# Kernel optimization log

Measured on AMD Instinct MI355X. Metric: run time of the kernel, lower is better.

Reference implementation:

```python
import jax, jax.numpy as jnp
import numpy as np

B, T = 32, 64
C, H, W = 1, 32, 32
A, E, D, S, HID = 2, 64, 128, 32, 128
K, STRIDE, PAD = 4, 2, 1
FEAT = 64 * 4 * 4  # conv stack output: 64 channels at 4x4


def _lin(x, w, b):
    return x @ w.T + b


def _conv(x, w, b):
    y = jax.lax.conv_general_dilated(x, w, (STRIDE, STRIDE), [(PAD, PAD)] * 2,
                                     dimension_numbers=('NCHW', 'OIHW', 'NCHW'))
    return y + b[None, :, None, None]


def _deconv(x, w, b):
    # torch ConvTranspose2d(w: (in_c,out_c,k,k), stride=2, pad=1) as dilated conv
    w_ = jnp.flip(w, (2, 3)).transpose(1, 0, 2, 3)
    p = K - 1 - PAD
    y = jax.lax.conv_general_dilated(x, w_, (1, 1), [(p, p)] * 2,
                                     lhs_dilation=(STRIDE, STRIDE),
                                     dimension_numbers=('NCHW', 'OIHW', 'NCHW'))
    return y + b[None, :, None, None]


def _mlp(x, w1, b1, w2, b2, w3, b3):
    h = jax.nn.elu(_lin(x, w1, b1))
    h = jax.nn.elu(_lin(h, w2, b2))
    out = _lin(h, w3, b3)
    return out[..., :S], jnp.clip(out[..., S:], -5.0, 2.0)


def _gru(x, h, wih, whh, bih, bhh):
    # torch nn.GRUCell semantics
    gi = x @ wih.T + bih
    gh = h @ whh.T + bhh
    ir, iz, inn = jnp.split(gi, 3, -1)
    hr, hz, hn = jnp.split(gh, 3, -1)
    r = jax.nn.sigmoid(ir + hr)
    u = jax.nn.sigmoid(iz + hz)
    n = jnp.tanh(inn + r * hn)
    return (1.0 - u) * n + u * h


def setup_inputs():
    keys = iter(jax.random.split(jax.random.key(0), 64))

    def p(shape, fan):
        return jax.random.normal(next(keys), shape, jnp.float32) / np.sqrt(fan)

    return dict(
        obs=jax.random.normal(next(keys), (B, T, C, H, W), jnp.float32),
        actions=jax.random.normal(next(keys), (B, T, A), jnp.float32),
        noise=jax.random.normal(next(keys), (T, B, S), jnp.float32),
        enc_w1=p((32, C, K, K), C * K * K), enc_b1=jnp.zeros(32),
        enc_w2=p((64, 32, K, K), 32 * K * K), enc_b2=jnp.zeros(64),
        enc_w3=p((64, 64, K, K), 64 * K * K), enc_b3=jnp.zeros(64),
        enc_pw=p((E, FEAT), FEAT), enc_pb=jnp.zeros(E),
        dec_pw=p((FEAT, D + S), D + S), dec_pb=jnp.zeros(FEAT),
        dec_w1=p((64, 64, K, K), 64 * K * K), dec_b1=jnp.zeros(64),
        dec_w2=p((64, 32, K, K), 64 * K * K), dec_b2=jnp.zeros(32),
        dec_w3=p((32, C, K, K), 32 * K * K), dec_b3=jnp.zeros(C),
        gru_wih=p((3 * D, S + A), D), gru_whh=p((3 * D, D), D),
        gru_bih=jnp.zeros(3 * D), gru_bhh=jnp.zeros(3 * D),
        pri_w1=p((HID, D + A), D + A), pri_b1=jnp.zeros(HID),
        pri_w2=p((HID, HID), HID), pri_b2=jnp.zeros(HID),
        pri_w3=p((2 * S, HID), HID), pri_b3=jnp.zeros(2 * S),
        pos_w1=p((HID, D + E), D + E), pos_b1=jnp.zeros(HID),
        pos_w2=p((HID, HID), HID), pos_b2=jnp.zeros(HID),
        pos_w3=p((2 * S, HID), HID), pos_b3=jnp.zeros(2 * S),
    )


def reference(obs, actions, noise, enc_w1, enc_b1, enc_w2, enc_b2, enc_w3, enc_b3,
              enc_pw, enc_pb, dec_pw, dec_pb, dec_w1, dec_b1, dec_w2, dec_b2,
              dec_w3, dec_b3, gru_wih, gru_whh, gru_bih, gru_bhh,
              pri_w1, pri_b1, pri_w2, pri_b2, pri_w3, pri_b3,
              pos_w1, pos_b1, pos_w2, pos_b2, pos_w3, pos_b3):
    Bq, Tq = obs.shape[:2]
    # --- CNN encoder over all frames at once ---
    x = obs.reshape(Bq * Tq, C, H, W)
    x = jax.nn.relu(_conv(x, enc_w1, enc_b1))
    x = jax.nn.relu(_conv(x, enc_w2, enc_b2))
    x = jax.nn.relu(_conv(x, enc_w3, enc_b3))
    embed = _lin(x.reshape(Bq * Tq, -1), enc_pw, enc_pb).reshape(Bq, Tq, E)

    # --- sequential RSSM core (use_posterior=True path) ---
    def step(h, inp):
        a, e_t, eps = inp
        pm, pls = _mlp(jnp.concatenate([h, e_t], -1),
                       pos_w1, pos_b1, pos_w2, pos_b2, pos_w3, pos_b3)
        z = pm + jnp.exp(pls) * eps
        prm, prls = _mlp(jnp.concatenate([h, a], -1),
                         pri_w1, pri_b1, pri_w2, pri_b2, pri_w3, pri_b3)
        h_new = _gru(jnp.concatenate([z, a], -1), h, gru_wih, gru_whh, gru_bih, gru_bhh)
        return h_new, (z, prm, prls, pm, pls, h)  # h = pre-update (used for decode)

    h0 = jnp.zeros((Bq, D), obs.dtype)
    h_final, (zs, prm, prls, pm, pls, hs) = jax.lax.scan(
        step, h0, (actions.swapaxes(0, 1), embed.swapaxes(0, 1), noise))

    # --- batched decode of all (h_t, z_t); same math as per-step decode ---
    hz = jnp.concatenate([hs, zs], -1).reshape(Tq * Bq, D + S)
    y = _lin(hz, dec_pw, dec_pb).reshape(Tq * Bq, 64, 4, 4)
    y = jax.nn.relu(_deconv(y, dec_w1, dec_b1))
    y = jax.nn.relu(_deconv(y, dec_w2, dec_b2))
    y = jax.nn.sigmoid(_deconv(y, dec_w3, dec_b3))
    recons = y.reshape(Tq, Bq, C, H, W).swapaxes(0, 1)

    tb = lambda t: t.swapaxes(0, 1)  # (T,B,.) -> (B,T,.)
    return (recons, tb(zs), tb(prm), tb(prls), tb(pm), tb(pls), h_final)
```

## Files before the change

### kernel.cpp

```cpp
#include <hip/hip_runtime.h>
#include <math.h>

#define NB 32
#define NT 64
#define NF 2048

#define OUT_ZS    2097152
#define OUT_PRM   (OUT_ZS + 65536)
#define OUT_PRLS  (OUT_PRM + 65536)
#define OUT_PM    (OUT_PRLS + 65536)
#define OUT_PLS   (OUT_PM + 65536)
#define OUT_HF    (OUT_PLS + 65536)

#define WS_HS    27394048
#define WS_ENCWF 27656192
#define WS_WP1H  27885568
#define WS_WP2   27893760
#define WS_WP3   27901952
#define WS_WWHH  27906048
#define WS_WIHZ  27930624
#define WS_PW1E  27977984
#define WS_WIHT  28002560
#define WS_WC2   16777216
#define WS_WC3   (WS_WC2 + 16384)
#define WS_WD1   (WS_WC3 + 32768)
#define WS_WD2   (WS_WD1 + 32768)
#define WS_DLIN  16908288
#define WS_DECWF 17960960
#define WS_QW1F  18045952
#define WS_QW2F  18057216
#define WS_QW3F  18066432
#define WS_XE    18874368
#define WS_POSL1E 25165824
#define WS_GIA    (WS_POSL1E + 262144)

typedef __attribute__((ext_vector_type(8))) short short8;
typedef __attribute__((ext_vector_type(4))) float floatx4;
typedef _Float16 __attribute__((ext_vector_type(2))) half2v;
typedef _Float16 __attribute__((ext_vector_type(8))) half8;
union U4S8 { uint4 u; short8 s; };
__device__ __forceinline__ short8 u2s(uint4 u) { U4S8 x; x.u = u; return x.s; }
union U4HH { uint4 u; half8 h; };
__device__ __forceinline__ half8 u2hh(uint4 u) { U4HH x; x.u = u; return x.h; }

__device__ __forceinline__ float rcpf(float x) {
#if __has_builtin(__builtin_amdgcn_rcpf)
  return __builtin_amdgcn_rcpf(x);
#else
  return 1.f / x;
#endif
}
__device__ __forceinline__ float eluf(float a) {
  return (a > 0.f) ? a : (__expf(a) - 1.f);
}
__device__ __forceinline__ float sigm(float a) {
  return rcpf(1.f + __expf(-a));
}
__device__ __forceinline__ float tanhfast(float x) {
  const float e = __expf(fminf(-2.f * x, 60.f));
  return (1.f - e) * rcpf(1.f + e);
}
__device__ __forceinline__ unsigned short f2bf(float f) {
  unsigned int u = __float_as_uint(f);
  u += 0x7fffu + ((u >> 16) & 1u);
  return (unsigned short)(u >> 16);
}
__device__ __forceinline__ unsigned short f2h(float f) {
  _Float16 h = (_Float16)f;
  return __builtin_bit_cast(unsigned short, h);
}
__device__ __forceinline__ unsigned int pack2h(float a, float b) {
  return (unsigned int)f2h(a) | ((unsigned int)f2h(b) << 16);
}
union UH2 { unsigned int u; half2v h; };
__device__ __forceinline__ half2v u2h(unsigned int u) { UH2 x; x.u = u; return x.h; }

__device__ __forceinline__ float fdot2w(half2v a, half2v b, float c) {
#if __has_builtin(__builtin_amdgcn_fdot2)
  return __builtin_amdgcn_fdot2(a, b, c, false);
#else
  return fmaf((float)a[0], (float)b[0], fmaf((float)a[1], (float)b[1], c));
#endif
}

union U4H2 { uint4 u; half2v h[4]; };
__device__ __forceinline__ void dot8h(uint4 w, uint4 x,
                                      float& a0, float& a1, float& a2, float& a3) {
  U4H2 W; W.u = w;
  U4H2 X; X.u = x;
  a0 = fdot2w(W.h[0], X.h[0], a0);
  a1 = fdot2w(W.h[1], X.h[1], a1);
  a2 = fdot2w(W.h[2], X.h[2], a2);
  a3 = fdot2w(W.h[3], X.h[3], a3);
}

struct PP { const float* src; void* dst; int n; int mode; int A; int B; };
struct PPAll { PP m[16]; };

__global__ __launch_bounds__(256) void k_prep(PPAll a) {
  PP p = a.m[blockIdx.y];
  for (int i = blockIdx.x * 256 + threadIdx.x; i < p.n; i += gridDim.x * 256) {
    if (p.mode == 10) {
      const int r = i / p.B, c = i - r * p.B;
      ((float*)p.dst)[c * p.A + r] = p.src[i];
    } else {
      float v;
      if (p.mode == 0) v = p.src[i];
      else if (p.mode == 1) v = p.src[(i >> 7) * 192 + (i & 127)];
      else if (p.mode == 2) v = p.src[(i >> 5) * 34 + (i & 31)];
      else if (p.mode == 6) {
        const int o = i / 160, k = i - o * 160;
        v = (k < 130) ? p.src[o * 130 + k] : 0.f;
      } else if (p.mode == 7) {
        v = p.src[(i >> 6) * 192 + 128 + (i & 63)];
      } else {
        const int ab = p.A * p.B;
        const int t = i / ab, rem = i - t * ab;
        const int oc = rem / p.B, ic = rem - oc * p.B;
        v = (p.mode == 3) ? p.src[(oc * p.B + ic) * 16 + t]
                          : p.src[(ic * p.A + oc) * 16 + t];
      }
      ((unsigned short*)p.dst)[i] = (p.mode <= 2 || p.mode >= 6) ? f2h(v) : f2bf(v);
    }
  }
}

__global__ __launch_bounds__(256, 3) void k_enc(
    const float* __restrict__ obs, const float* __restrict__ act,
    const float* __restrict__ w1, const float* __restrict__ b1,
    const unsigned short* __restrict__ wc2, const float* __restrict__ b2,
    const unsigned short* __restrict__ wc3, const float* __restrict__ b3,
    const float* __restrict__ wihT, const float* __restrict__ bih,
    const float* __restrict__ bhh,
    unsigned short* __restrict__ xe, float* __restrict__ gia) {
  const int f = blockIdx.x, tid = threadIdx.x;
  const int w = tid >> 6, l = tid & 63, q = l >> 4, n = l & 15;
  __shared__ float sIn1[32 * 33];
  __shared__ float sW1[512];
  __shared__ float sB1[32];
  __shared__ __align__(16) unsigned short sIn2[18 * 18 * 40];
  __shared__ __align__(16) unsigned short sIn3[10 * 10 * 72];
  __shared__ __align__(16) _Float16 sXeh[1024];
  __shared__ float sA2[2];

  {
    const float* in = obs + (size_t)f * 1024;
    for (int i = tid; i < 1024; i += 256) sIn1[(i >> 5) * 33 + (i & 31)] = in[i];
    for (int i = tid; i < 512; i += 256) sW1[i] = w1[i];
    if (tid < 32) sB1[tid] = b1[tid];
    if (tid < 2) sA2[tid] = act[(size_t)f * 2 + tid];
    unsigned int* z2 = (unsigned int*)sIn2;
    for (int i = tid; i < 18 * 18 * 40 / 2; i += 256) z2[i] = 0u;
    unsigned int* z3 = (unsigned int*)sIn3;
    for (int i = tid; i < 10 * 10 * 72 / 2; i += 256) z3[i] = 0u;
  }
  __syncthreads();
  for (int r = tid; r < 512; r += 256) {
    const int oc = r >> 4, oy = r & 15;
    float acc[16];
    const float bv = sB1[oc];
#pragma unroll
    for (int j = 0; j < 16; j++) acc[j] = bv;
#pragma unroll
    for (int ky = 0; ky < 4; ky++) {
      const int iy = 2 * oy + ky - 1;
      if (iy < 0 || iy >= 32) continue;
#pragma unroll
      for (int kx = 0; kx < 4; kx++) {
        const float wv = sW1[oc * 16 + ky * 4 + kx];
#pragma unroll
        for (int j = 0; j < 16; j++) {
          const int ix = 2 * j + kx - 1;
          if (ix >= 0 && ix < 32) acc[j] += wv * sIn1[iy * 33 + ix];
        }
      }
    }
#pragma unroll
    for (int j = 0; j < 16; j++)
      sIn2[((oy + 1) * 18 + (j + 1)) * 40 + oc] = f2bf(fmaxf(acc[j], 0.f));
  }
  __syncthreads();
  {
    int base[4];
#pragma unroll
    for (int nt = 0; nt < 4; nt++) {
      const int px = nt * 16 + n, oy = px >> 3, ox = px & 7;
      base[nt] = ((2 * oy + 1) * 18 + (2 * ox + 1)) * 40 + q * 8;
    }
    floatx4 acc[4];
#pragma unroll
    for (int nt = 0; nt < 4; nt++) acc[nt] = (floatx4){0.f, 0.f, 0.f, 0.f};
    uint4 af[16];
#pragma unroll
    for (int t = 0; t < 16; t++)
      af[t] = *reinterpret_cast<const uint4*>(wc2 + (size_t)(t * 64 + w * 16 + n) * 32 + q * 8);
#pragma unroll
    for (int t = 0; t < 16; t++) {
      const int toff = ((t / 4 - 1) * 18 + (t % 4 - 1)) * 40;
#pragma unroll
      for (int nt = 0; nt < 4; nt++) {
        uint4 bf = *reinterpret_cast<const uint4*>(&sIn2[base[nt] + toff]);
        acc[nt] = __builtin_amdgcn_mfma_f32_16x16x32_bf16(u2s(af[t]), u2s(bf), acc[nt], 0, 0, 0);
      }
    }
    float b4[4];
#pragma unroll
    for (int r = 0; r < 4; r++) b4[r] = b2[w * 16 + q * 4 + r];
    __syncthreads();
#pragma unroll
    for (int nt = 0; nt < 4; nt++) {
      const int px = nt * 16 + n, oy = px >> 3, ox = px & 7;
#pragma unroll
      for (int r = 0; r < 4; r++)
        sIn3[((oy + 1) * 10 + (ox + 1)) * 72 + (w * 16 + q * 4 + r)] =
            f2bf(fmaxf(acc[nt][r] + b4[r], 0.f));
    }
  }
  __syncthreads();
  {
    const int oy = n >> 2, ox = n & 3;
    const int ibase = ((2 * oy + 1) * 10 + (2 * ox + 1)) * 72 + q * 8;
    floatx4 acc = (floatx4){0.f, 0.f, 0.f, 0.f};
    for (int ks = 0; ks < 2; ks++) {
      uint4 af[16];
#pragma unroll
      for (int t = 0; t < 16; t++)
        af[t] = *reinterpret_cast<const uint4*>(
            wc3 + (size_t)(t * 64 + w * 16 + n) * 64 + ks * 32 + q * 8);
#pragma unroll
      for (int t = 0; t < 16; t++) {
        const int toff = ((t / 4 - 1) * 10 + (t % 4 - 1)) * 72 + ks * 32;
        uint4 bf = *reinterpret_cast<const uint4*>(&sIn3[ibase + toff]);
        acc = __builtin_amdgcn_mfma_f32_16x16x32_bf16(u2s(af[t]), u2s(bf), acc, 0, 0, 0);
      }
    }
#pragma unroll
    for (int r = 0; r < 4; r++) {
      const int ch = w * 16 + q * 4 + r;
      sXeh[ch * 16 + n] = (_Float16)fmaxf(acc[r] + b3[ch], 0.f);
    }
  }
  __syncthreads();
  *reinterpret_cast<uint2*>(&xe[(size_t)f * 1024 + tid * 4]) =
      *reinterpret_cast<const uint2*>(&sXeh[tid * 4]);
  if (tid >= 128) {
#pragma unroll
    for (int jj = 0; jj < 3; jj++) {
      const int j = (tid - 128) + jj * 128;
      gia[(size_t)f * 384 + (tid - 128) * 3 + jj] =
          bih[j] + bhh[j] + wihT[32 * 384 + j] * sA2[0] + wihT[33 * 384 + j] * sA2[1];
    }
  }
}

__global__ __launch_bounds__(256) void k_emb(
    const unsigned short* __restrict__ xe,
    const unsigned short* __restrict__ encwf, const float* __restrict__ encb,
    const unsigned short* __restrict__ pw1e, const float* __restrict__ pb1,
    float* __restrict__ posl1e) {
  const int tid = threadIdx.x;
  const int fBase = blockIdx.x * 16;
  const int w = tid >> 6, l = tid & 63, q = l >> 4, n = l & 15;
  __shared__ __align__(16) _Float16 sB[16][1032];
  __shared__ __align__(16) _Float16 sE2[16][72];
#pragma unroll
  for (int j = 0; j < 8; j++) {
    const int i4 = tid + j * 256;
    const int fr = i4 >> 7, kq = (i4 & 127) * 8;
    *reinterpret_cast<uint4*>(&sB[fr][kq]) =
        *reinterpret_cast<const uint4*>(&xe[(size_t)(fBase + fr) * 1024 + kq]);
  }
  __syncthreads();
  {
    const int oB = w * 16;
    floatx4 acc = (floatx4){0.f, 0.f, 0.f, 0.f};
#pragma unroll
    for (int ks = 0; ks < 32; ks++) {
      uint4 a = *reinterpret_cast<const uint4*>(
          &encwf[(size_t)(oB + n) * 1024 + ks * 32 + q * 8]);
      uint4 bb = *reinterpret_cast<const uint4*>(&sB[n][ks * 32 + q * 8]);
      acc = __builtin_amdgcn_mfma_f32_16x16x32_f16(u2hh(a), u2hh(bb), acc, 0, 0, 0);
    }
    const int o0 = oB + q * 4;
    *reinterpret_cast<unsigned int*>(&sE2[n][o0]) =
        pack2h(acc[0] + encb[o0], acc[1] + encb[o0 + 1]);
    *reinterpret_cast<unsigned int*>(&sE2[n][o0 + 2]) =
        pack2h(acc[2] + encb[o0 + 2], acc[3] + encb[o0 + 3]);
  }
  __syncthreads();
#pragma unroll
  for (int g = 0; g < 2; g++) {
    const int oB = g * 64 + w * 16;
    floatx4 acc = (floatx4){0.f, 0.f, 0.f, 0.f};
#pragma unroll
    for (int ks = 0; ks < 2; ks++) {
      uint4 a = *reinterpret_cast<const uint4*>(&pw1e[(oB + n) * 64 + ks * 32 + q * 8]);
      uint4 bb = *reinterpret_cast<const uint4*>(&sE2[n][ks * 32 + q * 8]);
      acc = __builtin_amdgcn_mfma_f32_16x16x32_f16(u2hh(a), u2hh(bb), acc, 0, 0, 0);
    }
    const int o0 = oB + q * 4;
#pragma unroll
    for (int r = 0; r < 4; r++)
      posl1e[(size_t)(fBase + n) * 128 + o0 + r] = acc[r] + pb1[o0 + r];
  }
}

__global__ __launch_bounds__(512, 2) void k_rssm4(
    const float* __restrict__ posl1e, const float* __restrict__ gia,
    const float* __restrict__ noise,
    const unsigned short* __restrict__ wp1h, const unsigned short* __restrict__ wp2,
    const unsigned short* __restrict__ wp3, const unsigned short* __restrict__ wwhh,
    const unsigned short* __restrict__ wihz,
    const float* __restrict__ pb2, const float* __restrict__ pb3,
    float* __restrict__ hs, float* __restrict__ out) {
  const int b = blockIdx.x, tid = threadIdx.x;
  const int R = tid >> 2, ks4 = tid & 3;
  __shared__ __align__(16) _Float16 sHh[128];
  __shared__ __align__(16) _Float16 sL1h[128];
  __shared__ __align__(16) _Float16 sL2h[128];
  __shared__ __align__(16) _Float16 sZh[32];
  __shared__ float sGh[384];

  uint4 wA4[4][4];
  {
#pragma unroll
    for (int j = 0; j < 4; j++) {
      const unsigned short* p = (j == 0)
          ? (wp1h + R * 128)
          : (wwhh + (size_t)((j - 1) * 128 + R) * 128);
      const uint4* pv = reinterpret_cast<const uint4*>(p + ks4 * 32);
#pragma unroll
      for (int i = 0; i < 4; i++) wA4[j][i] = pv[i];
    }
  }
  uint4 wB[4];
  {
    const unsigned short* rowB = wp2 + R * 128 + ks4 * 32;
#pragma unroll
    for (int i = 0; i < 4; i++) wB[i] = reinterpret_cast<const uint4*>(rowB)[i];
  }
  uint4 wC[2];
  {
    const int r = tid >> 3;
    const int o = (r >> 1) + ((r & 1) << 5);
    const unsigned short* rowC = wp3 + o * 128 + (tid & 7) * 16;
#pragma unroll
    for (int i = 0; i < 2; i++) wC[i] = reinterpret_cast<const uint4*>(rowC)[i];
  }
  uint4 wD[3][4];
  if (tid < 128) {
#pragma unroll
    for (int j = 0; j < 3; j++) {
      const unsigned short* rowD = wihz + (size_t)(tid + 128 * j) * 32;
#pragma unroll
      for (int i = 0; i < 4; i++) wD[j][i] = reinterpret_cast<const uint4*>(rowD)[i];
    }
  }
  const bool zlane = (tid & 15) == 0;
  const int jz = tid >> 4;
  const float pb2R = pb2[R];
  const float pb3mR = zlane ? pb3[jz] : 0.f;
  const float pb3sR = zlane ? pb3[jz + 32] : 0.f;

  float h_reg = 0.f;
  float pl1R = 0.f, epsR = 0.f;
  float3 gaR = {0.f, 0.f, 0.f};
  if (ks4 == 0) pl1R = posl1e[(size_t)(b * 64) * 128 + R];
  if (tid < 128) {
    gaR = *reinterpret_cast<const float3*>(&gia[(size_t)(b * 64) * 384 + tid * 3]);
    sHh[tid] = (_Float16)0.f;
    hs[(size_t)b * 128 + tid] = 0.f;
  }
  if (zlane) epsR = noise[(size_t)b * 32 + jz];
  __syncthreads();

  for (int t = 0; t < 64; ++t) {
    const int tn = (t < 63) ? t + 1 : 63;
    float pl1N = 0.f, epsN = 0.f;
    float3 gaN = {0.f, 0.f, 0.f};
    if (ks4 == 0) pl1N = posl1e[(size_t)(b * 64 + tn) * 128 + R];
    if (tid < 128)
      gaN = *reinterpret_cast<const float3*>(&gia[(size_t)(b * 64 + tn) * 384 + tid * 3]);
    if (zlane) epsN = noise[(size_t)(tn * 32 + b) * 32 + jz];

    {
      const uint4* xs = reinterpret_cast<const uint4*>(sHh) + ks4 * 4;
      const uint4 x0 = xs[0], x1 = xs[1], x2 = xs[2], x3 = xs[3];
      float part[4];
#pragma unroll
      for (int j = 0; j < 4; j++) {
        float p0 = 0.f, p1 = 0.f, p2 = 0.f, p3 = 0.f;
        dot8h(wA4[j][0], x0, p0, p1, p2, p3);
        dot8h(wA4[j][1], x1, p0, p1, p2, p3);
        dot8h(wA4[j][2], x2, p0, p1, p2, p3);
        dot8h(wA4[j][3], x3, p0, p1, p2, p3);
        part[j] = (p0 + p1) + (p2 + p3);
      }
#pragma unroll
      for (int j = 0; j < 4; j++) {
        part[j] += __shfl_xor(part[j], 1);
        part[j] += __shfl_xor(part[j], 2);
      }
      if (ks4 == 0) {
        sL1h[R] = (_Float16)eluf(part[0] + pl1R);
        sGh[R * 3] = part[1];
        sGh[R * 3 + 1] = part[2];
        sGh[R * 3 + 2] = part[3];
      }
    }
    __syncthreads();
    {
      float a0 = 0.f, a1 = 0.f, a2 = 0.f, a3 = 0.f;
      const uint4* xs = reinterpret_cast<const uint4*>(sL1h) + ks4 * 4;
#pragma unroll
      for (int i = 0; i < 4; i++) dot8h(wB[i], xs[i], a0, a1, a2, a3);
      float p = (a0 + a1) + (a2 + a3);
      p += __shfl_xor(p, 1);
      p += __shfl_xor(p, 2);
      if (ks4 == 0) sL2h[R] = (_Float16)eluf(p + pb2R);
    }
    __syncthreads();
    {
      float a0 = 0.f, a1 = 0.f, a2 = 0.f, a3 = 0.f;
      const uint4* xs = reinterpret_cast<const uint4*>(sL2h) + (tid & 7) * 2;
      dot8h(wC[0], xs[0], a0, a1, a2, a3);
      dot8h(wC[1], xs[1], a0, a1, a2, a3);
      float p = (a0 + a1) + (a2 + a3);
      p += __shfl_xor(p, 1);
      p += __shfl_xor(p, 2);
      p += __shfl_xor(p, 4);
      const float pq = __shfl_xor(p, 8);
      if (zlane) {
        const float pm = p + pb3mR;
        float pls = pq + pb3sR;
        pls = fminf(fmaxf(pls, -5.f), 2.f);
        const float z = pm + __expf(pls) * epsR;
        sZh[jz] = (_Float16)z;
        const int o = (b * 64 + t) * 32 + jz;
        out[OUT_ZS + o] = z;
        out[OUT_PM + o] = pm;
        out[OUT_PLS + o] = pls;
      }
    }
    __syncthreads();
    if (tid < 128) {
      float r0 = 0.f, r1 = 0.f, r2 = 0.f, r3 = 0.f;
      float u0 = 0.f, u1 = 0.f, u2 = 0.f, u3 = 0.f;
      float m0 = 0.f, m1 = 0.f, m2 = 0.f, m3 = 0.f;
      const uint4* xs = reinterpret_cast<const uint4*>(sZh);
#pragma unroll
      for (int i = 0; i < 4; i++) {
        const uint4 xv = xs[i];
        dot8h(wD[0][i], xv, r0, r1, r2, r3);
        dot8h(wD[1][i], xv, u0, u1, u2, u3);
        dot8h(wD[2][i], xv, m0, m1, m2, m3);
      }
      const float gr = gaR.x + ((r0 + r1) + (r2 + r3));
      const float gu = gaR.y + ((u0 + u1) + (u2 + u3));
      const float gn = gaR.z + ((m0 + m1) + (m2 + m3));
      const float ghr = sGh[tid * 3];
      const float ghu = sGh[tid * 3 + 1];
      const float ghn = sGh[tid * 3 + 2];
      const float r = sigm(gr + ghr);
      const float u = sigm(gu + ghu);
      const float n = tanhfast(gn + r * ghn);
      const float hn = (1.f - u) * n + u * h_reg;
      h_reg = hn;
      sHh[tid] = (_Float16)hn;
      if (t < 63) hs[(size_t)((t + 1) * 32 + b) * 128 + tid] = hn;
    }
    pl1R = pl1N;
    gaR = gaN;
    epsR = epsN;
    __syncthreads();
  }
  if (tid < 128) out[OUT_HF + b * 128 + tid] = h_reg;
}

__global__ __launch_bounds__(256) void k_post(
    const float* __restrict__ hs, const float* __restrict__ zs,
    const unsigned short* __restrict__ decwf, const float* __restrict__ decb,
    unsigned short* __restrict__ dlin,
    const float* __restrict__ act,
    const unsigned short* __restrict__ qw1f, const float* __restrict__ qb1,
    const unsigned short* __restrict__ qw2f, const float* __restrict__ qb2,
    const unsigned short* __restrict__ qw3f, const float* __restrict__ qb3,
    float* __restrict__ out) {
  const int tid = threadIdx.x;
  const int bid = blockIdx.x;
  const int w = tid >> 6, l = tid & 63, q = l >> 4, n = l & 15;
  __shared__ __align__(16) _Float16 sB[16][168];
  __shared__ __align__(16) _Float16 sB2[16][136];

  if (bid < 2048) {
    const int otile = bid & 15;
    const int fBase = (bid >> 4) * 16;
    for (int i = tid; i < 2560; i += 256) {
      const int fr = i / 160, k = i - fr * 160;
      const int f = fBase + fr;
      float v;
      if (k < 128) v = hs[(size_t)f * 128 + k];
      else v = zs[(size_t)((f & 31) * 64 + (f >> 5)) * 32 + (k - 128)];
      sB[fr][k] = (_Float16)v;
    }
    __syncthreads();
    const int oB = otile * 64 + w * 16;
    floatx4 acc = (floatx4){0.f, 0.f, 0.f, 0.f};
#pragma unroll
    for (int ks = 0; ks < 5; ks++) {
      uint4 a = *reinterpret_cast<const uint4*>(&decwf[(size_t)(oB + n) * 160 + ks * 32 + q * 8]);
      uint4 bb = *reinterpret_cast<const uint4*>(&sB[n][ks * 32 + q * 8]);
      acc = __builtin_amdgcn_mfma_f32_16x16x32_f16(u2hh(a), u2hh(bb), acc, 0, 0, 0);
    }
    const int o0 = oB + q * 4;
    const int f = fBase + n;
    const unsigned int lo = (unsigned int)f2bf(acc[0] + decb[o0]) |
                            ((unsigned int)f2bf(acc[1] + decb[o0 + 1]) << 16);
    const unsigned int hi = (unsigned int)f2bf(acc[2] + decb[o0 + 2]) |
                            ((unsigned int)f2bf(acc[3] + decb[o0 + 3]) << 16);
    *reinterpret_cast<uint2*>(&dlin[(size_t)f * 1024 + o0]) = make_uint2(lo, hi);
    return;
  }
  const int fBase = (bid - 2048) * 16;
  for (int i = tid; i < 2560; i += 256) {
    const int fr = i / 160, k = i - fr * 160;
    const int f = fBase + fr;
    float v = 0.f;
    if (k < 128) v = hs[(size_t)f * 128 + k];
    else if (k < 130) v = act[(size_t)((f & 31) * 64 + (f >> 5)) * 2 + (k - 128)];
    sB[fr][k] = (_Float16)v;
  }
  __syncthreads();
#pragma unroll
  for (int g = 0; g < 2; g++) {
    const int oB = g * 64 + w * 16;
    floatx4 acc = (floatx4){0.f, 0.f, 0.f, 0.f};
#pragma unroll
    for (int ks = 0; ks < 5; ks++) {
      uint4 a = *reinterpret_cast<const uint4*>(&qw1f[(oB + n) * 160 + ks * 32 + q * 8]);
      uint4 bb = *reinterpret_cast<const uint4*>(&sB[n][ks * 32 + q * 8]);
      acc = __builtin_amdgcn_mfma_f32_16x16x32_f16(u2hh(a), u2hh(bb), acc, 0, 0, 0);
    }
    const int o0 = oB + q * 4;
    *reinterpret_cast<unsigned int*>(&sB2[n][o0]) =
        pack2h(eluf(acc[0] + qb1[o0]), eluf(acc[1] + qb1[o0 + 1]));
    *reinterpret_cast<unsigned int*>(&sB2[n][o0 + 2]) =
        pack2h(eluf(acc[2] + qb1[o0 + 2]), eluf(acc[3] + qb1[o0 + 3]));
  }
  __syncthreads();
#pragma unroll
  for (int g = 0; g < 2; g++) {
    const int oB = g * 64 + w * 16;
    floatx4 acc = (floatx4){0.f, 0.f, 0.f, 0.f};
#pragma unroll
    for (int ks = 0; ks < 4; ks++) {
      uint4 a = *reinterpret_cast<const uint4*>(&qw2f[(oB + n) * 128 + ks * 32 + q * 8]);
      uint4 bb = *reinterpret_cast<const uint4*>(&sB2[n][ks * 32 + q * 8]);
      acc = __builtin_amdgcn_mfma_f32_16x16x32_f16(u2hh(a), u2hh(bb), acc, 0, 0, 0);
    }
    const int o0 = oB + q * 4;
    *reinterpret_cast<unsigned int*>(&sB[n][o0]) =
        pack2h(eluf(acc[0] + qb2[o0]), eluf(acc[1] + qb2[o0 + 1]));
    *reinterpret_cast<unsigned int*>(&sB[n][o0 + 2]) =
        pack2h(eluf(acc[2] + qb2[o0 + 2]), eluf(acc[3] + qb2[o0 + 3]));
  }
  __syncthreads();
  {
    const int oB = w * 16;
    floatx4 acc = (floatx4){0.f, 0.f, 0.f, 0.f};
#pragma unroll
    for (int ks = 0; ks < 4; ks++) {
      uint4 a = *reinterpret_cast<const uint4*>(&qw3f[(oB + n) * 128 + ks * 32 + q * 8]);
      uint4 bb = *reinterpret_cast<const uint4*>(&sB[n][ks * 32 + q * 8]);
      acc = __builtin_amdgcn_mfma_f32_16x16x32_f16(u2hh(a), u2hh(bb), acc, 0, 0, 0);
    }
    const int o0 = oB + q * 4;
    const int f = fBase + n;
    const int ob = ((f & 31) * 64 + (f >> 5)) * 32;
#pragma unroll
    for (int r = 0; r < 4; r++) {
      const int o = o0 + r;
      const float v = acc[r] + qb3[o];
      if (o < 32) out[OUT_PRM + ob + o] = v;
      else out[OUT_PRLS + ob + o - 32] = fminf(fmaxf(v, -5.f), 2.f);
    }
  }
}

#define D3_ROW 580
#define D3_PX  36
__global__ __launch_bounds__(256, 4) void k_dec(
    const unsigned short* __restrict__ dlin,
    const unsigned short* __restrict__ wd1, const float* __restrict__ db1,
    const unsigned short* __restrict__ wd2, const float* __restrict__ db2,
    const float* __restrict__ w3, const float* __restrict__ b3,
    float* __restrict__ out) {
  const int f = blockIdx.x, tid = threadIdx.x;
  const int w = tid >> 6, l = tid & 63, q = l >> 4, n = l & 15;
  const int t = f >> 5, b = f & 31;
  __shared__ __align__(16) unsigned short sInD1[6 * 6 * 72];
  __shared__ __align__(16) unsigned short sInD2[10 * 10 * 72];
  __shared__ __align__(16) _Float16 sInD3h[16 * D3_ROW];
  __shared__ __align__(16) _Float16 sW3h[16 * 32];

  const uint2 dv = *reinterpret_cast<const uint2*>(dlin + (size_t)f * 1024 + tid * 4);
  {
    unsigned int* z1 = (unsigned int*)sInD1;
    for (int i = tid; i < 6 * 6 * 72 / 2; i += 256) z1[i] = 0u;
    unsigned int* z2 = (unsigned int*)sInD2;
    for (int i = tid; i < 10 * 10 * 72 / 2; i += 256) z2[i] = 0u;
    for (int s = tid; s < 512; s += 256) {
      const int tap = s >> 5, icc = s & 31;
      sW3h[s] = (_Float16)w3[icc * 16 + tap];
    }
  }
  __syncthreads();
  {
    const int o0 = tid * 4, c = o0 >> 4, px0 = o0 & 15;
    const int Y = px0 >> 2;
    const int base = ((Y + 1) * 6 + 1) * 72 + c;
    sInD1[base] = (unsigned short)(dv.x & 0xffffu);
    sInD1[base + 72] = (unsigned short)(dv.x >> 16);
    sInD1[base + 144] = (unsigned short)(dv.y & 0xffffu);
    sInD1[base + 216] = (unsigned short)(dv.y >> 16);
  }
  __syncthreads();
  {
    const int Y = n >> 2, X = n & 3;
    const int ibase = ((Y + 1) * 6 + (X + 1)) * 72 + q * 8;
    float b4[4];
#pragma unroll
    for (int r = 0; r < 4; r++) b4[r] = db1[w * 16 + q * 4 + r];
#pragma unroll
    for (int c = 0; c < 4; c++) {
      const int cy = c >> 1, cx = c & 1;
      floatx4 acc = (floatx4){0.f, 0.f, 0.f, 0.f};
      for (int ks = 0; ks < 2; ks++) {
        uint4 af[4];
#pragma unroll
        for (int tt = 0; tt < 4; tt++) {
          const int t2 = tt >> 1, t3 = tt & 1;
          const int ky = ((cy + 1) & 1) + 2 * t2, kx = ((cx + 1) & 1) + 2 * t3;
          af[tt] = *reinterpret_cast<const uint4*>(
              wd1 + (size_t)((ky * 4 + kx) * 64 + w * 16 + n) * 64 + ks * 32 + q * 8);
        }
#pragma unroll
        for (int tt = 0; tt < 4; tt++) {
          const int t2 = tt >> 1, t3 = tt & 1;
          const int toff = ((cy - t2) * 6 + (cx - t3)) * 72 + ks * 32;
          uint4 bf = *reinterpret_cast<const uint4*>(&sInD1[ibase + toff]);
          acc = __builtin_amdgcn_mfma_f32_16x16x32_bf16(u2s(af[tt]), u2s(bf), acc, 0, 0, 0);
        }
      }
      const int oy = 2 * Y + cy, ox = 2 * X + cx;
#pragma unroll
      for (int r = 0; r < 4; r++)
        sInD2[((oy + 1) * 10 + (ox + 1)) * 72 + (w * 16 + q * 4 + r)] =
            f2bf(fmaxf(acc[r] + b4[r], 0.f));
    }
  }
  __syncthreads();
  {
    const int px = w * 16 + n;
    const int Y = px >> 3, X = px & 7;
    const int ibase = ((Y + 1) * 10 + (X + 1)) * 72 + q * 8;
    float b4[2][4];
#pragma unroll
    for (int mi = 0; mi < 2; mi++)
#pragma unroll
      for (int r = 0; r < 4; r++) b4[mi][r] = db2[mi * 16 + q * 4 + r];
#pragma unroll
    for (int c = 0; c < 4; c++) {
      const int cy = c >> 1, cx = c & 1;
      floatx4 acc[2];
      acc[0] = (floatx4){0.f, 0.f, 0.f, 0.f};
      acc[1] = (floatx4){0.f, 0.f, 0.f, 0.f};
      for (int ks = 0; ks < 2; ks++) {
        uint4 af[2][4];
#pragma unroll
        for (int mi = 0; mi < 2; mi++)
#pragma unroll
          for (int tt = 0; tt < 4; tt++) {
            const int t2 = tt >> 1, t3 = tt & 1;
            const int ky = ((cy + 1) & 1) + 2 * t2, kx = ((cx + 1) & 1) + 2 * t3;
            af[mi][tt] = *reinterpret_cast<const uint4*>(
                wd2 + (size_t)((ky * 4 + kx) * 32 + mi * 16 + n) * 64 + ks * 32 + q * 8);
          }
#pragma unroll
        for (int tt = 0; tt < 4; tt++) {
          const int t2 = tt >> 1, t3 = tt & 1;
          const int toff = ((cy - t2) * 10 + (cx - t3)) * 72 + ks * 32;
          uint4 bf = *reinterpret_cast<const uint4*>(&sInD2[ibase + toff]);
#pragma unroll
          for (int mi = 0; mi < 2; mi++)
            acc[mi] = __builtin_amdgcn_mfma_f32_16x16x32_bf16(u2s(af[mi][tt]), u2s(bf),
                                                              acc[mi], 0, 0, 0);
        }
      }
      const int oy = 2 * Y + cy, ox = 2 * X + cx;
#pragma unroll
      for (int mi = 0; mi < 2; mi++) {
        const unsigned int lo =
            (unsigned int)f2h(fmaxf(acc[mi][0] + b4[mi][0], 0.f)) |
            ((unsigned int)f2h(fmaxf(acc[mi][1] + b4[mi][1], 0.f)) << 16);
        const unsigned int hi =
            (unsigned int)f2h(fmaxf(acc[mi][2] + b4[mi][2], 0.f)) |
            ((unsigned int)f2h(fmaxf(acc[mi][3] + b4[mi][3], 0.f)) << 16);
        *reinterpret_cast<uint2*>(&sInD3h[oy * D3_ROW + ox * D3_PX + mi * 16 + q * 4]) =
            make_uint2(lo, hi);
      }
    }
  }
  __syncthreads();
  {
    const int oy = tid >> 3;
    const int rem2 = tid & 7;
    const int cpar = rem2 >> 2, qq = rem2 & 3;
    const int py = (oy + 1) & 1, pc = (cpar + 1) & 1;
    const int ixb0 = (cpar + 1 - pc) >> 1;
    const int xlo = ixb0 - 1 + qq * 4;
    float acc[4] = {0.f, 0.f, 0.f, 0.f};
    const float bv = b3[0];
#pragma unroll
    for (int u2 = 0; u2 < 2; u2++) {
      const int ky = py + 2 * u2;
      const int iy = (oy + 1 - ky) >> 1;
      if (iy < 0 || iy >= 16) continue;
      const _Float16* rowp = &sInD3h[iy * D3_ROW];
      const uint2* wAp = reinterpret_cast<const uint2*>(&sW3h[(ky * 4 + pc) * 32]);
      const uint2* wBp = reinterpret_cast<const uint2*>(&sW3h[(ky * 4 + pc + 2) * 32]);
#pragma unroll
      for (int kb = 0; kb < 8; kb++) {
        uint2 xv[5];
#pragma unroll
        for (int x = 0; x < 5; x++) {
          const int ix = xlo + x;
          xv[x] = (ix >= 0 && ix < 16)
              ? *reinterpret_cast<const uint2*>(&rowp[ix * D3_PX + kb * 4])
              : make_uint2(0u, 0u);
        }
        const uint2 wa = wAp[kb], wb = wBp[kb];
#pragma unroll
        for (int j = 0; j < 4; j++) {
          acc[j] = fdot2w(u2h(wa.x), u2h(xv[j + 1].x), acc[j]);
          acc[j] = fdot2w(u2h(wa.y), u2h(xv[j + 1].y), acc[j]);
          acc[j] = fdot2w(u2h(wb.x), u2h(xv[j].x), acc[j]);
          acc[j] = fdot2w(u2h(wb.y), u2h(xv[j].y), acc[j]);
        }
      }
    }
    const int fo = b * 64 + t;
    float* yf = out + (size_t)fo * 1024;
#pragma unroll
    for (int j = 0; j < 4; j++)
      yf[oy * 32 + (cpar + 2 * (qq * 4 + j))] = rcpf(1.f + __expf(-(acc[j] + bv)));
  }
}

extern "C" void kernel_launch(void* const* d_in, const int* in_sizes, int n_in,
                              void* d_out, int out_size, void* d_ws, size_t ws_size,
                              hipStream_t stream) {
  const float* obs = (const float*)d_in[0];
  const float* actions = (const float*)d_in[1];
  const float* noise = (const float*)d_in[2];
  const float* enc_w1 = (const float*)d_in[3];
  const float* enc_b1 = (const float*)d_in[4];
  const float* enc_w2 = (const float*)d_in[5];
  const float* enc_b2 = (const float*)d_in[6];
  const float* enc_w3 = (const float*)d_in[7];
  const float* enc_b3 = (const float*)d_in[8];
  const float* enc_pw = (const float*)d_in[9];
  const float* enc_pb = (const float*)d_in[10];
  const float* dec_pw = (const float*)d_in[11];
  const float* dec_pb = (const float*)d_in[12];
  const float* dec_w1 = (const float*)d_in[13];
  const float* dec_b1 = (const float*)d_in[14];
  const float* dec_w2 = (const float*)d_in[15];
  const float* dec_b2 = (const float*)d_in[16];
  const float* dec_w3 = (const float*)d_in[17];
  const float* dec_b3 = (const float*)d_in[18];
  const float* gru_wih = (const float*)d_in[19];
  const float* gru_whh = (const float*)d_in[20];
  const float* gru_bih = (const float*)d_in[21];
  const float* gru_bhh = (const float*)d_in[22];
  const float* pri_w1 = (const float*)d_in[23];
  const float* pri_b1 = (const float*)d_in[24];
  const float* pri_w2 = (const float*)d_in[25];
  const float* pri_b2 = (const float*)d_in[26];
  const float* pri_w3 = (const float*)d_in[27];
  const float* pri_b3 = (const float*)d_in[28];
  const float* pos_w1 = (const float*)d_in[29];
  const float* pos_b1 = (const float*)d_in[30];
  const float* pos_w2 = (const float*)d_in[31];
  const float* pos_b2 = (const float*)d_in[32];
  const float* pos_w3 = (const float*)d_in[33];
  const float* pos_b3 = (const float*)d_in[34];

  float* out = (float*)d_out;
  float* ws = (float*)d_ws;
  float* HS = ws + WS_HS;
  float* POSL1E = ws + WS_POSL1E;
  float* GIA = ws + WS_GIA;
  unsigned short* WP1H = (unsigned short*)(ws + WS_WP1H);
  unsigned short* WP2 = (unsigned short*)(ws + WS_WP2);
  unsigned short* WP3 = (unsigned short*)(ws + WS_WP3);
  unsigned short* WWHH = (unsigned short*)(ws + WS_WWHH);
  unsigned short* WIHZ = (unsigned short*)(ws + WS_WIHZ);
  unsigned short* WC2 = (unsigned short*)(ws + WS_WC2);
  unsigned short* WC3 = (unsigned short*)(ws + WS_WC3);
  unsigned short* WD1 = (unsigned short*)(ws + WS_WD1);
  unsigned short* WD2 = (unsigned short*)(ws + WS_WD2);
  unsigned short* DLIN = (unsigned short*)(ws + WS_DLIN);
  unsigned short* DECWF = (unsigned short*)(ws + WS_DECWF);
  unsigned short* QW1F = (unsigned short*)(ws + WS_QW1F);
  unsigned short* QW2F = (unsigned short*)(ws + WS_QW2F);
  unsigned short* QW3F = (unsigned short*)(ws + WS_QW3F);
  unsigned short* ENCWF = (unsigned short*)(ws + WS_ENCWF);
  unsigned short* PW1E = (unsigned short*)(ws + WS_PW1E);
  unsigned short* XE = (unsigned short*)(ws + WS_XE);

  PPAll pp;
  pp.m[0]  = {enc_pw, ENCWF, 64 * 1024, 0, 0, 0};
  pp.m[1]  = {dec_pw, DECWF, 1024 * 160, 0, 0, 0};
  pp.m[2]  = {pri_w1, QW1F, 128 * 160, 6, 0, 0};
  pp.m[3]  = {pri_w2, QW2F, 128 * 128, 0, 0, 0};
  pp.m[4]  = {pri_w3, QW3F, 64 * 128, 0, 0, 0};
  pp.m[5]  = {pos_w1, PW1E, 128 * 64, 7, 0, 0};
  pp.m[6]  = {gru_wih, ws + WS_WIHT, 384 * 34, 10, 384, 34};
  pp.m[7]  = {pos_w1, WP1H, 128 * 128, 1, 0, 0};
  pp.m[8]  = {pos_w2, WP2, 128 * 128, 0, 0, 0};
  pp.m[9]  = {pos_w3, WP3, 64 * 128, 0, 0, 0};
  pp.m[10] = {gru_whh, WWHH, 384 * 128, 0, 0, 0};
  pp.m[11] = {gru_wih, WIHZ, 384 * 32, 2, 0, 0};
  pp.m[12] = {enc_w2, WC2, 16 * 64 * 32, 3, 64, 32};
  pp.m[13] = {enc_w3, WC3, 16 * 64 * 64, 3, 64, 64};
  pp.m[14] = {dec_w1, WD1, 16 * 64 * 64, 4, 64, 64};
  pp.m[15] = {dec_w2, WD2, 16 * 32 * 64, 4, 32, 64};
  hipLaunchKernelGGL(k_prep, dim3(32, 16), dim3(256), 0, stream, pp);

  k_enc<<<NF, 256, 0, stream>>>(obs, actions, enc_w1, enc_b1, WC2, enc_b2,
                                WC3, enc_b3, ws + WS_WIHT, gru_bih, gru_bhh,
                                XE, GIA);

  k_emb<<<128, 256, 0, stream>>>(XE, ENCWF, enc_pb, PW1E, pos_b1, POSL1E);

  k_rssm4<<<NB, 512, 0, stream>>>(POSL1E, GIA, noise, WP1H, WP2, WP3, WWHH, WIHZ,
                                  pos_b2, pos_b3, HS, out);

  k_post<<<2176, 256, 0, stream>>>(HS, out + OUT_ZS, DECWF, dec_pb, DLIN,
                                   actions, QW1F, pri_b1, QW2F, pri_b2,
                                   QW3F, pri_b3, out);

  k_dec<<<NF, 256, 0, stream>>>(DLIN, WD1, dec_b1, WD2, dec_b2, dec_w3, dec_b3, out);
}
```

Before: 434.5 us.

## Compute posterior output layer redundantly per GRU wave to drop a block barrier

The posterior MLP's third layer now runs in each of the two GRU waves, with each lane computing a full 128-wide dot product for one output row. Each wave writes z to its own shared buffer and needs only a wave barrier, which removes one block-wide __syncthreads per timestep. Launch bounds drop to one block per SM to fit the larger register footprint of holding full wp3 rows (16 uint4 per thread). The cost is duplicated work, longer serial dot products per lane, and lower occupancy.

Measured after the change: 437.8 us. No clear change (+0.8%).

```diff
diff --git a/kernel.cpp b/kernel.cpp
--- a/kernel.cpp
+++ b/kernel.cpp
@@ -305,7 +305,7 @@
   }
 }
 
-__global__ __launch_bounds__(512, 2) void k_rssm4(
+__global__ __launch_bounds__(512, 1) void k_rssm4(
     const float* __restrict__ posl1e, const float* __restrict__ gia,
     const float* __restrict__ noise,
     const unsigned short* __restrict__ wp1h, const unsigned short* __restrict__ wp2,
@@ -315,10 +315,11 @@
     float* __restrict__ hs, float* __restrict__ out) {
   const int b = blockIdx.x, tid = threadIdx.x;
   const int R = tid >> 2, ks4 = tid & 3;
+  const int lane = tid & 63;
   __shared__ __align__(16) _Float16 sHh[128];
   __shared__ __align__(16) _Float16 sL1h[128];
   __shared__ __align__(16) _Float16 sL2h[128];
-  __shared__ __align__(16) _Float16 sZh[32];
+  __shared__ __align__(16) _Float16 sZw[2][32];
   __shared__ float sGh[384];
 
   uint4 wA4[4][4];
@@ -339,13 +340,11 @@
 #pragma unroll
     for (int i = 0; i < 4; i++) wB[i] = reinterpret_cast<const uint4*>(rowB)[i];
   }
-  uint4 wC[2];
-  {
-    const int r = tid >> 3;
-    const int o = (r >> 1) + ((r & 1) << 5);
-    const unsigned short* rowC = wp3 + o * 128 + (tid & 7) * 16;
-#pragma unroll
-    for (int i = 0; i < 2; i++) wC[i] = reinterpret_cast<const uint4*>(rowC)[i];
+  uint4 wC8[16];
+  {
+    const uint4* rowC = reinterpret_cast<const uint4*>(wp3 + lane * 128);
+#pragma unroll
+    for (int i = 0; i < 16; i++) wC8[i] = rowC[i];
   }
   uint4 wD[3][4];
   if (tid < 128) {
@@ -356,11 +355,8 @@
       for (int i = 0; i < 4; i++) wD[j][i] = reinterpret_cast<const uint4*>(rowD)[i];
     }
   }
-  const bool zlane = (tid & 15) == 0;
-  const int jz = tid >> 4;
   const float pb2R = pb2[R];
-  const float pb3mR = zlane ? pb3[jz] : 0.f;
-  const float pb3sR = zlane ? pb3[jz + 32] : 0.f;
+  const float pb3R = pb3[lane];
 
   float h_reg = 0.f;
   float pl1R = 0.f, epsR = 0.f;
@@ -370,8 +366,8 @@
     gaR = *reinterpret_cast<const float3*>(&gia[(size_t)(b * 64) * 384 + tid * 3]);
     sHh[tid] = (_Float16)0.f;
     hs[(size_t)b * 128 + tid] = 0.f;
-  }
-  if (zlane) epsR = noise[(size_t)b * 32 + jz];
+    epsR = noise[(size_t)b * 32 + (tid & 31)];
+  }
   __syncthreads();
 
   for (int t = 0; t < 64; ++t) {
@@ -379,9 +375,10 @@
     float pl1N = 0.f, epsN = 0.f;
     float3 gaN = {0.f, 0.f, 0.f};
     if (ks4 == 0) pl1N = posl1e[(size_t)(b * 64 + tn) * 128 + R];
-    if (tid < 128)
+    if (tid < 128) {
       gaN = *reinterpret_cast<const float3*>(&gia[(size_t)(b * 64 + tn) * 384 + tid * 3]);
-    if (zlane) epsN = noise[(size_t)(tn * 32 + b) * 32 + jz];
+      epsN = noise[(size_t)(tn * 32 + b) * 32 + (tid & 31)];
+    }
 
     {
       const uint4* xs = reinterpret_cast<const uint4*>(sHh) + ks4 * 4;
@@ -420,37 +417,34 @@
       if (ks4 == 0) sL2h[R] = (_Float16)eluf(p + pb2R);
     }
     __syncthreads();
-    {
+    if (tid < 128) {
+      const int w01 = tid >> 6;
       float a0 = 0.f, a1 = 0.f, a2 = 0.f, a3 = 0.f;
-      const uint4* xs = reinterpret_cast<const uint4*>(sL2h) + (tid & 7) * 2;
-      dot8h(wC[0], xs[0], a0, a1, a2, a3);
-      dot8h(wC[1], xs[1], a0, a1, a2, a3);
-      float p = (a0 + a1) + (a2 + a3);
-      p += __shfl_xor(p, 1);
-      p += __shfl_xor(p, 2);
-      p += __shfl_xor(p, 4);
-      const float pq = __shfl_xor(p, 8);
-      if (zlane) {
-        const float pm = p + pb3mR;
-        float pls = pq + pb3sR;
-        pls = fminf(fmaxf(pls, -5.f), 2.f);
+      const uint4* xs = reinterpret_cast<const uint4*>(sL2h);
+#pragma unroll
+      for (int i = 0; i < 16; i++) dot8h(wC8[i], xs[i], a0, a1, a2, a3);
+      const float p = (a0 + a1) + (a2 + a3) + pb3R;
+      const float pq = __shfl_xor(p, 32);
+      if (lane < 32) {
+        const float pm = p;
+        float pls = fminf(fmaxf(pq, -5.f), 2.f);
         const float z = pm + __expf(pls) * epsR;
-        sZh[jz] = (_Float16)z;
-        const int o = (b * 64 + t) * 32 + jz;
-        out[OUT_ZS + o] = z;
-        out[OUT_PM + o] = pm;
-        out[OUT_PLS + o] = pls;
-      }
-    }
-    __syncthreads();
-    if (tid < 128) {
+        sZw[w01][lane] = (_Float16)z;
+        if (tid < 32) {
+          const int o = (b * 64 + t) * 32 + lane;
+          out[OUT_ZS + o] = z;
+          out[OUT_PM + o] = pm;
+          out[OUT_PLS + o] = pls;
+        }
+      }
+      __builtin_amdgcn_wave_barrier();
       float r0 = 0.f, r1 = 0.f, r2 = 0.f, r3 = 0.f;
       float u0 = 0.f, u1 = 0.f, u2 = 0.f, u3 = 0.f;
       float m0 = 0.f, m1 = 0.f, m2 = 0.f, m3 = 0.f;
-      const uint4* xs = reinterpret_cast<const uint4*>(sZh);
+      const uint4* zs4 = reinterpret_cast<const uint4*>(sZw[w01]);
 #pragma unroll
       for (int i = 0; i < 4; i++) {
-        const uint4 xv = xs[i];
+        const uint4 xv = zs4[i];
         dot8h(wD[0][i], xv, r0, r1, r2, r3);
         dot8h(wD[1][i], xv, u0, u1, u2, u3);
         dot8h(wD[2][i], xv, m0, m1, m2, m3);
```

## Fuse embedding projection kernel into the RSSM recurrence kernel prologue

Applied to the files above, without the earlier changes.

Removes the separate k_emb launch and computes each batch's 64 timesteps of encoder projection plus posterior first-layer input term inside k_rssm4's prologue. The results go into shared memory instead of a global scratch buffer, which saves a kernel launch and a global round trip, and per-step loads inside the serial loop now come from LDS. In exchange, the 32 RSSM blocks do this GEMM work on only 32 CUs instead of 128 blocks, and shared memory use grows to about 100KB per block. Launch bounds drop to one block per SM.

Result: slower. 456.7 us (+5.1%).

```diff
diff --git a/kernel.cpp b/kernel.cpp
--- a/kernel.cpp
+++ b/kernel.cpp
@@ -31,8 +31,7 @@
 #define WS_QW2F  18057216
 #define WS_QW3F  18066432
 #define WS_XE    18874368
-#define WS_POSL1E 25165824
-#define WS_GIA    (WS_POSL1E + 262144)
+#define WS_GIA   25165824
 
 typedef __attribute__((ext_vector_type(8))) short short8;
 typedef __attribute__((ext_vector_type(4))) float floatx4;
@@ -253,61 +252,11 @@
   }
 }
 
-__global__ __launch_bounds__(256) void k_emb(
+__global__ __launch_bounds__(512, 1) void k_rssm4(
     const unsigned short* __restrict__ xe,
     const unsigned short* __restrict__ encwf, const float* __restrict__ encb,
     const unsigned short* __restrict__ pw1e, const float* __restrict__ pb1,
-    float* __restrict__ posl1e) {
-  const int tid = threadIdx.x;
-  const int fBase = blockIdx.x * 16;
-  const int w = tid >> 6, l = tid & 63, q = l >> 4, n = l & 15;
-  __shared__ __align__(16) _Float16 sB[16][1032];
-  __shared__ __align__(16) _Float16 sE2[16][72];
-#pragma unroll
-  for (int j = 0; j < 8; j++) {
-    const int i4 = tid + j * 256;
-    const int fr = i4 >> 7, kq = (i4 & 127) * 8;
-    *reinterpret_cast<uint4*>(&sB[fr][kq]) =
-        *reinterpret_cast<const uint4*>(&xe[(size_t)(fBase + fr) * 1024 + kq]);
-  }
-  __syncthreads();
-  {
-    const int oB = w * 16;
-    floatx4 acc = (floatx4){0.f, 0.f, 0.f, 0.f};
-#pragma unroll
-    for (int ks = 0; ks < 32; ks++) {
-      uint4 a = *reinterpret_cast<const uint4*>(
-          &encwf[(size_t)(oB + n) * 1024 + ks * 32 + q * 8]);
-      uint4 bb = *reinterpret_cast<const uint4*>(&sB[n][ks * 32 + q * 8]);
-      acc = __builtin_amdgcn_mfma_f32_16x16x32_f16(u2hh(a), u2hh(bb), acc, 0, 0, 0);
-    }
-    const int o0 = oB + q * 4;
-    *reinterpret_cast<unsigned int*>(&sE2[n][o0]) =
-        pack2h(acc[0] + encb[o0], acc[1] + encb[o0 + 1]);
-    *reinterpret_cast<unsigned int*>(&sE2[n][o0 + 2]) =
-        pack2h(acc[2] + encb[o0 + 2], acc[3] + encb[o0 + 3]);
-  }
-  __syncthreads();
-#pragma unroll
-  for (int g = 0; g < 2; g++) {
-    const int oB = g * 64 + w * 16;
-    floatx4 acc = (floatx4){0.f, 0.f, 0.f, 0.f};
-#pragma unroll
-    for (int ks = 0; ks < 2; ks++) {
-      uint4 a = *reinterpret_cast<const uint4*>(&pw1e[(oB + n) * 64 + ks * 32 + q * 8]);
-      uint4 bb = *reinterpret_cast<const uint4*>(&sE2[n][ks * 32 + q * 8]);
-      acc = __builtin_amdgcn_mfma_f32_16x16x32_f16(u2hh(a), u2hh(bb), acc, 0, 0, 0);
-    }
-    const int o0 = oB + q * 4;
-#pragma unroll
-    for (int r = 0; r < 4; r++)
-      posl1e[(size_t)(fBase + n) * 128 + o0 + r] = acc[r] + pb1[o0 + r];
-  }
-}
-
-__global__ __launch_bounds__(512, 2) void k_rssm4(
-    const float* __restrict__ posl1e, const float* __restrict__ gia,
-    const float* __restrict__ noise,
+    const float* __restrict__ gia, const float* __restrict__ noise,
     const unsigned short* __restrict__ wp1h, const unsigned short* __restrict__ wp2,
     const unsigned short* __restrict__ wp3, const unsigned short* __restrict__ wwhh,
     const unsigned short* __restrict__ wihz,
@@ -315,12 +264,67 @@
     float* __restrict__ hs, float* __restrict__ out) {
   const int b = blockIdx.x, tid = threadIdx.x;
   const int R = tid >> 2, ks4 = tid & 3;
+  __shared__ __align__(16) _Float16 sB[2][16][1032];
+  __shared__ __align__(16) _Float16 sE2[2][16][72];
+  __shared__ float sPL[64][128];
   __shared__ __align__(16) _Float16 sHh[128];
   __shared__ __align__(16) _Float16 sL1h[128];
   __shared__ __align__(16) _Float16 sL2h[128];
   __shared__ __align__(16) _Float16 sZh[32];
   __shared__ float sGh[384];
 
+  {
+    const int half = tid >> 8;
+    const int htid = tid & 255;
+    const int hw = htid >> 6, hl = htid & 63, hq = hl >> 4, hn = hl & 15;
+#pragma unroll
+    for (int pair = 0; pair < 2; pair++) {
+      const int fBase = b * 64 + pair * 32 + half * 16;
+#pragma unroll
+      for (int j = 0; j < 8; j++) {
+        const int i4 = htid + j * 256;
+        const int fr = i4 >> 7, kq = (i4 & 127) * 8;
+        *reinterpret_cast<uint4*>(&sB[half][fr][kq]) =
+            *reinterpret_cast<const uint4*>(&xe[(size_t)(fBase + fr) * 1024 + kq]);
+      }
+      __syncthreads();
+      {
+        const int oB = hw * 16;
+        floatx4 acc = (floatx4){0.f, 0.f, 0.f, 0.f};
+#pragma unroll
+        for (int ks = 0; ks < 32; ks++) {
+          uint4 a = *reinterpret_cast<const uint4*>(
+              &encwf[(size_t)(oB + hn) * 1024 + ks * 32 + hq * 8]);
+          uint4 bb = *reinterpret_cast<const uint4*>(&sB[half][hn][ks * 32 + hq * 8]);
+          acc = __builtin_amdgcn_mfma_f32_16x16x32_f16(u2hh(a), u2hh(bb), acc, 0, 0, 0);
+        }
+        const int o0 = oB + hq * 4;
+        *reinterpret_cast<unsigned int*>(&sE2[half][hn][o0]) =
+            pack2h(acc[0] + encb[o0], acc[1] + encb[o0 + 1]);
+        *reinterpret_cast<unsigned int*>(&sE2[half][hn][o0 + 2]) =
+            pack2h(acc[2] + encb[o0 + 2], acc[3] + encb[o0 + 3]);
+      }
+      __syncthreads();
+#pragma unroll
+      for (int g = 0; g < 2; g++) {
+        const int oB = g * 64 + hw * 16;
+        floatx4 acc = (floatx4){0.f, 0.f, 0.f, 0.f};
+#pragma unroll
+        for (int ks = 0; ks < 2; ks++) {
+          uint4 a = *reinterpret_cast<const uint4*>(&pw1e[(oB + hn) * 64 + ks * 32 + hq * 8]);
+          uint4 bb = *reinterpret_cast<const uint4*>(&sE2[half][hn][ks * 32 + hq * 8]);
+          acc = __builtin_amdgcn_mfma_f32_16x16x32_f16(u2hh(a), u2hh(bb), acc, 0, 0, 0);
+        }
+        const int o0 = oB + hq * 4;
+        const int tloc = pair * 32 + half * 16 + hn;
+#pragma unroll
+        for (int r = 0; r < 4; r++)
+          sPL[tloc][o0 + r] = acc[r] + pb1[o0 + r];
+      }
+    }
+  }
+  __syncthreads();
+
   uint4 wA4[4][4];
   {
 #pragma unroll
@@ -365,7 +369,7 @@
   float h_reg = 0.f;
   float pl1R = 0.f, epsR = 0.f;
   float3 gaR = {0.f, 0.f, 0.f};
-  if (ks4 == 0) pl1R = posl1e[(size_t)(b * 64) * 128 + R];
+  if (ks4 == 0) pl1R = sPL[0][R];
   if (tid < 128) {
     gaR = *reinterpret_cast<const float3*>(&gia[(size_t)(b * 64) * 384 + tid * 3]);
     sHh[tid] = (_Float16)0.f;
@@ -378,7 +382,7 @@
     const int tn = (t < 63) ? t + 1 : 63;
     float pl1N = 0.f, epsN = 0.f;
     float3 gaN = {0.f, 0.f, 0.f};
-    if (ks4 == 0) pl1N = posl1e[(size_t)(b * 64 + tn) * 128 + R];
+    if (ks4 == 0) pl1N = sPL[tn][R];
     if (tid < 128)
       gaN = *reinterpret_cast<const float3*>(&gia[(size_t)(b * 64 + tn) * 384 + tid * 3]);
     if (zlane) epsN = noise[(size_t)(tn * 32 + b) * 32 + jz];
@@ -799,7 +803,6 @@
   float* out = (float*)d_out;
   float* ws = (float*)d_ws;
   float* HS = ws + WS_HS;
-  float* POSL1E = ws + WS_POSL1E;
   float* GIA = ws + WS_GIA;
   unsigned short* WP1H = (unsigned short*)(ws + WS_WP1H);
   unsigned short* WP2 = (unsigned short*)(ws + WS_WP2);
@@ -842,9 +845,8 @@
                                 WC3, enc_b3, ws + WS_WIHT, gru_bih, gru_bhh,
                                 XE, GIA);
 
-  k_emb<<<128, 256, 0, stream>>>(XE, ENCWF, enc_pb, PW1E, pos_b1, POSL1E);
-
-  k_rssm4<<<NB, 512, 0, stream>>>(POSL1E, GIA, noise, WP1H, WP2, WP3, WWHH, WIHZ,
+  k_rssm4<<<NB, 512, 0, stream>>>(XE, ENCWF, enc_pb, PW1E, pos_b1,
+                                  GIA, noise, WP1H, WP2, WP3, WWHH, WIHZ,
                                   pos_b2, pos_b3, HS, out);
 
   k_post<<<2176, 256, 0, stream>>>(HS, out + OUT_ZS, DECWF, dec_pb, DLIN,
```
